# Optimization experiments

Hardware: AMD Instinct MI355X
Metric: run time of the kernel (lower is better)

Reference implementation:

```python
import jax, jax.numpy as jnp
import numpy as np

N = 20000
E = 320000
IN_C = 256
HID = 64
OUT_C = 64
NUM_LAYERS = 3
HEADS = 8


def setup_inputs() -> dict:
    key = jax.random.key(0)
    ks = jax.random.split(key, 12)
    s_in = 1.0 / np.sqrt(IN_C)
    s_h = 1.0 / np.sqrt(HID)
    inp = {
        "x": jax.random.normal(ks[0], (N, IN_C), dtype=jnp.float32),
        "edge_index": jax.random.randint(ks[1], (2, E), 0, N, dtype=jnp.int64),
        "lin1_w": jax.random.uniform(ks[2], (IN_C, HID), jnp.float32, -s_in, s_in),
        "lin1_b": jnp.zeros((HID,), jnp.float32),
        "wq": jax.random.uniform(ks[3], (NUM_LAYERS, HID, HID), jnp.float32, -s_h, s_h),
        "bq": jnp.zeros((NUM_LAYERS, HID), jnp.float32),
        "wk": jax.random.uniform(ks[4], (NUM_LAYERS, HID, HID), jnp.float32, -s_h, s_h),
        "bk": jnp.zeros((NUM_LAYERS, HID), jnp.float32),
        "wv": jax.random.uniform(ks[5], (NUM_LAYERS, HID, HID), jnp.float32, -s_h, s_h),
        "bv": jnp.zeros((NUM_LAYERS, HID), jnp.float32),
        "lin2_w": jax.random.uniform(ks[6], (HID, OUT_C), jnp.float32, -s_h, s_h),
        "lin2_b": jnp.zeros((OUT_C,), jnp.float32),
    }
    return inp


def reference(x, edge_index, lin1_w, lin1_b, wq, bq, wk, bk, wv, bv, lin2_w, lin2_b):
    n = x.shape[0]
    C = lin1_w.shape[1]
    d = C // HEADS  # per-head dim
    inv_sqrt_d = 1.0 / (d ** 0.5)

    # gcn_norm with self-loops (symmetric normalization, edge weights = 1)
    loop = jnp.arange(n, dtype=edge_index.dtype)
    row = jnp.concatenate([edge_index[0], loop])  # source j
    col = jnp.concatenate([edge_index[1], loop])  # target i
    deg = jax.ops.segment_sum(jnp.ones_like(col, dtype=x.dtype), col, num_segments=n)
    dinv = jnp.where(deg > 0, deg ** -0.5, 0.0)
    norm = dinv[row] * dinv[col]  # [E+N]

    # input projection (dropout inactive in eval mode)
    h = jax.nn.relu(x @ lin1_w + lin1_b)
    x_all = h[:, None, :]  # [N, 1, C] growing history

    for l in range(NUM_LAYERS):
        t = x_all.shape[1]
        # node-level projections (linear commutes with gather)
        q = x_all[:, -1] @ wq[l] + bq[l]                      # [N, C]
        k = jnp.einsum("ntc,cd->ntd", x_all, wk[l]) + bk[l]   # [N, t, C]
        v = jnp.einsum("ntc,cd->ntd", x_all, wv[l]) + bv[l]   # [N, t, C]
        # per-edge multi-head attention of target's latest repr over source history
        Qe = q[col].reshape(-1, HEADS, d)                      # [E', H, d]
        Ke = k[row].reshape(-1, t, HEADS, d)                   # [E', t, H, d]
        Ve = v[row].reshape(-1, t, HEADS, d)
        scores = jnp.einsum("ehd,ethd->eht", Qe, Ke) * inv_sqrt_d
        attn = jax.nn.softmax(scores, axis=-1)                 # [E', H, t]
        msg = jnp.einsum("eht,ethd->ehd", attn, Ve).reshape(-1, C)
        msg = msg * norm[:, None]
        out = jax.ops.segment_sum(msg, col, num_segments=n)    # sum aggregation
        out = jax.nn.relu(out)
        x_all = jnp.concatenate([x_all, out[:, None, :]], axis=1)

    logits = x_all[:, -1] @ lin2_w + lin2_b
    return jax.nn.log_softmax(logits, axis=1)
```

## Files before the change

### kernel.cpp

```cpp
#include <hip/hip_runtime.h>
#include <math.h>

#define HID 64
#define HEADS 8
#define ALD 72

typedef __attribute__((ext_vector_type(8))) short bf16x8;
typedef __attribute__((ext_vector_type(4))) float f32x4;

__device__ __forceinline__ unsigned short f2bf(float f) {
    union { float f; unsigned int u; } cv; cv.f = f;
    unsigned int u = cv.u;
    unsigned int r = (u + 0x7FFFu + ((u >> 16) & 1u)) >> 16;
    return (unsigned short)r;
}
__device__ __forceinline__ float bflo(unsigned int u) {
    union { unsigned int u; float f; } cv; cv.u = u << 16; return cv.f;
}
__device__ __forceinline__ float bfhi(unsigned int u) {
    union { unsigned int u; float f; } cv; cv.u = u & 0xFFFF0000u; return cv.f;
}
__device__ __forceinline__ unsigned relu_pk(unsigned u) {
    unsigned m = ((u & 0x8000u) ? 0u : 0xFFFFu) |
                 ((u & 0x80000000u) ? 0u : 0xFFFF0000u);
    return u & m;
}

__device__ __forceinline__ float dot8(const float* qp, uint4 u) {
    return qp[0] * bflo(u.x) + qp[1] * bfhi(u.x) + qp[2] * bflo(u.y) +
           qp[3] * bfhi(u.y) + qp[4] * bflo(u.z) + qp[5] * bfhi(u.z) +
           qp[6] * bflo(u.w) + qp[7] * bfhi(u.w);
}
__device__ __forceinline__ void axpy8(float a, uint4 u, float* Y) {
    Y[0] += a * bflo(u.x); Y[1] += a * bfhi(u.x);
    Y[2] += a * bflo(u.y); Y[3] += a * bfhi(u.y);
    Y[4] += a * bflo(u.z); Y[5] += a * bfhi(u.z);
    Y[6] += a * bflo(u.w); Y[7] += a * bfhi(u.w);
}

__global__ void k_count(const int* __restrict__ col, int* __restrict__ counts, int E) {
    int e = blockIdx.x * blockDim.x + threadIdx.x;
    if (e < E) atomicAdd(&counts[col[e]], 1);
}

__global__ __launch_bounds__(1024) void k_scan(const int* __restrict__ counts,
                                               int* __restrict__ start,
                                               float* __restrict__ dinv, int n) {
    __shared__ int wsum[16];
    int tid = threadIdx.x;
    int lane = tid & 63, wvi = tid >> 6;
    int ipt = (n + 1023) >> 10;
    int c0 = tid * ipt;
    int c1 = min(n, c0 + ipt);
    int s = 0;
    for (int i = c0; i < c1; ++i) s += counts[i];
    int x = s;
#pragma unroll
    for (int off = 1; off < 64; off <<= 1) {
        int y = __shfl_up(x, off);
        if (lane >= off) x += y;
    }
    if (lane == 63) wsum[wvi] = x;
    __syncthreads();
    if (wvi == 0 && lane < 16) {
        int t2 = wsum[lane];
#pragma unroll
        for (int off = 1; off < 16; off <<= 1) {
            int y = __shfl_up(t2, off);
            if (lane >= off) t2 += y;
        }
        wsum[lane] = t2;
    }
    __syncthreads();
    int waveoff = (wvi > 0) ? wsum[wvi - 1] : 0;
    int run = waveoff + x - s;
    for (int i = c0; i < c1; ++i) {
        int v = counts[i];
        start[i] = run;
        dinv[i] = rsqrtf((float)(v + 1));
        run += v;
    }
    if (tid == 0) start[n] = wsum[15];
}

__global__ void k_scatter(const int* __restrict__ ei, const int* __restrict__ start,
                          int* __restrict__ counts, unsigned short* __restrict__ ebuf,
                          int E) {
    int e = blockIdx.x * blockDim.x + threadIdx.x;
    if (e >= E) return;
    int r = ei[e], c = ei[E + e];
    int pos = start[c] + atomicSub(&counts[c], 1) - 1;
    ebuf[pos] = (unsigned short)r;
}

__device__ __forceinline__ void stage_w_bf16(unsigned short* Wt,
                                             const float* __restrict__ w, int tid) {
    for (int idx = tid; idx < 1024; idx += 256) {
        int k = idx >> 4, n4 = (idx & 15) * 4;
        float4 wv = *(const float4*)&w[k * 64 + n4];
        Wt[(n4 + 0) * ALD + k] = f2bf(wv.x);
        Wt[(n4 + 1) * ALD + k] = f2bf(wv.y);
        Wt[(n4 + 2) * ALD + k] = f2bf(wv.z);
        Wt[(n4 + 3) * ALD + k] = f2bf(wv.w);
    }
}

__device__ __forceinline__ void mfma_step(const unsigned short* Alds,
                                          const unsigned short* Wt,
                                          int tid, f32x4 acc[4]) {
    int lane = tid & 63;
    int m0 = (tid >> 6) * 16;
    int c16 = lane & 15, quad = lane >> 4;
    const unsigned short* ar = &Alds[(m0 + c16) * ALD + quad * 8];
    bf16x8 a0 = *(const bf16x8*)ar;
    bf16x8 a1 = *(const bf16x8*)(ar + 32);
#pragma unroll
    for (int nt = 0; nt < 4; ++nt) {
        const unsigned short* br = &Wt[(nt * 16 + c16) * ALD + quad * 8];
        bf16x8 b0 = *(const bf16x8*)br;
        bf16x8 b1 = *(const bf16x8*)(br + 32);
        acc[nt] = __builtin_amdgcn_mfma_f32_16x16x32_bf16(a0, b0, acc[nt], 0, 0, 0);
        acc[nt] = __builtin_amdgcn_mfma_f32_16x16x32_bf16(a1, b1, acc[nt], 0, 0, 0);
    }
}

__global__ __launch_bounds__(256, 4) void k_lin1(
    const float* __restrict__ x, const float* __restrict__ w,
    const float* __restrict__ b, const float* __restrict__ wv0,
    const float* __restrict__ bv0, unsigned short* __restrict__ h,
    unsigned short* __restrict__ kv, int n) {
    __shared__ __align__(16) unsigned short Alds[64 * ALD];
    __shared__ __align__(16) unsigned short Wt[64 * ALD];
    int tid = threadIdx.x;
    int node0 = blockIdx.x * 64;
    f32x4 acc[4];
#pragma unroll
    for (int nt = 0; nt < 4; ++nt) acc[nt] = (f32x4){0.f, 0.f, 0.f, 0.f};

    for (int kc = 0; kc < 256; kc += 64) {
        __syncthreads();
        stage_w_bf16(Wt, w + kc * 64, tid);
        for (int idx = tid; idx < 1024; idx += 256) {
            int r = idx >> 4, c4 = (idx & 15) * 4;
            int node = node0 + r;
            float4 v = make_float4(0.f, 0.f, 0.f, 0.f);
            if (node < n) v = *(const float4*)&x[(size_t)node * 256 + kc + c4];
            Alds[r * ALD + c4 + 0] = f2bf(v.x);
            Alds[r * ALD + c4 + 1] = f2bf(v.y);
            Alds[r * ALD + c4 + 2] = f2bf(v.z);
            Alds[r * ALD + c4 + 3] = f2bf(v.w);
        }
        __syncthreads();
        mfma_step(Alds, Wt, tid, acc);
    }
    int lane = tid & 63;
    int m0 = (tid >> 6) * 16, c16 = lane & 15, quad = lane >> 4;
    float bias[4];
#pragma unroll
    for (int nt = 0; nt < 4; ++nt) bias[nt] = b[nt * 16 + c16];

    __syncthreads();
    stage_w_bf16(Wt, wv0, tid);
#pragma unroll
    for (int i = 0; i < 4; ++i) {
        int row = m0 + quad * 4 + i;
        int node = node0 + row;
#pragma unroll
        for (int nt = 0; nt < 4; ++nt) {
            unsigned short hb = f2bf(fmaxf(acc[nt][i] + bias[nt], 0.f));
            Alds[row * ALD + nt * 16 + c16] = hb;
            if (node < n) h[(size_t)node * 64 + nt * 16 + c16] = hb;
        }
    }
    __syncthreads();
    f32x4 acc2[4];
#pragma unroll
    for (int nt = 0; nt < 4; ++nt) acc2[nt] = (f32x4){0.f, 0.f, 0.f, 0.f};
    mfma_step(Alds, Wt, tid, acc2);
    float bias2[4];
#pragma unroll
    for (int nt = 0; nt < 4; ++nt) bias2[nt] = bv0[nt * 16 + c16];
#pragma unroll
    for (int i = 0; i < 4; ++i) {
        int node = node0 + m0 + quad * 4 + i;
        if (node < n) {
#pragma unroll
            for (int nt = 0; nt < 4; ++nt)
                kv[(size_t)node * 64 + nt * 16 + c16] = f2bf(acc2[nt][i] + bias2[nt]);
        }
    }
}

__global__ __launch_bounds__(256, 4) void k_stage(
    const unsigned short* __restrict__ xs, size_t sstride,
    const float* __restrict__ wk, const float* __restrict__ bk,
    const float* __restrict__ wv, const float* __restrict__ bv,
    unsigned short* __restrict__ kv1, unsigned short* __restrict__ kv2,
    int n, int phase) {
    int j = blockIdx.y;
    int layer, s, isV;
    if (phase == 0) { layer = 1; s = j & 1; isV = j >> 1; }
    else            { layer = 2; s = j >> 1; isV = j & 1; }
    const unsigned short* src = xs + (size_t)s * sstride;
    const float* w = (isV ? wv : wk) + layer * 4096;
    const float* b = (isV ? bv : bk) + layer * 64;
    unsigned short* dst = (layer == 1) ? kv1 : kv2;
    int stride = (layer == 1) ? 256 : 384;
    int koff = s * 128 + (isV ? 64 : 0);
    bool relu_in = (s >= 1);

    __shared__ __align__(16) unsigned short Alds[64 * ALD];
    __shared__ __align__(16) unsigned short Wt[64 * ALD];
    int tid = threadIdx.x;
    int node0 = blockIdx.x * 64;
    stage_w_bf16(Wt, w, tid);
    for (int idx = tid; idx < 512; idx += 256) {
        int r = idx >> 3, seg = idx & 7;
        int node = node0 + r;
        uint4 u = make_uint4(0u, 0u, 0u, 0u);
        if (node < n) u = *(const uint4*)&src[(size_t)node * 64 + seg * 8];
        if (relu_in) {
            u.x = relu_pk(u.x); u.y = relu_pk(u.y);
            u.z = relu_pk(u.z); u.w = relu_pk(u.w);
        }
        *(uint4*)&Alds[r * ALD + seg * 8] = u;
    }
    __syncthreads();
    f32x4 acc[4];
#pragma unroll
    for (int nt = 0; nt < 4; ++nt) acc[nt] = (f32x4){0.f, 0.f, 0.f, 0.f};
    mfma_step(Alds, Wt, tid, acc);

    int lane = tid & 63;
    int m0 = (tid >> 6) * 16, c16 = lane & 15, quad = lane >> 4;
    float bias[4];
#pragma unroll
    for (int nt = 0; nt < 4; ++nt) bias[nt] = b[nt * 16 + c16];
#pragma unroll
    for (int i = 0; i < 4; ++i) {
        int node = node0 + m0 + quad * 4 + i;
        if (node < n) {
#pragma unroll
            for (int nt = 0; nt < 4; ++nt)
                dst[(size_t)node * stride + koff + nt * 16 + c16] =
                    f2bf(acc[nt][i] + bias[nt]);
        }
    }
}

template <int T, bool FINAL>
__global__ __launch_bounds__(256) void k_attn(
    const int* __restrict__ start, const unsigned short* __restrict__ ebuf,
    const float* __restrict__ dinv, const unsigned short* __restrict__ xs,
    size_t sstride, const unsigned short* __restrict__ kv,
    const float* __restrict__ wq, const float* __restrict__ bq,
    const float* __restrict__ w2, const float* __restrict__ b2,
    unsigned short* __restrict__ outb, float* __restrict__ outf, int n) {
    const int KVS = (T == 1) ? 64 : T * 128;
    int node = (int)((blockIdx.x * (size_t)blockDim.x + threadIdx.x) >> 6);
    int lane = threadIdx.x & 63;
    if (node >= n) return;
    int g = lane >> 3;
    int cb = (lane & 7) * 8;

    float qv[8];
    if (T > 1) {
        const float isd = 0.35355339059327373f;
        const unsigned short* xrow =
            &xs[(size_t)(T - 1) * sstride + (size_t)node * 64];
        float a0 = 0.f, a1 = 0.f, a2 = 0.f, a3 = 0.f;
        float a4 = 0.f, a5 = 0.f, a6 = 0.f, a7 = 0.f;
#pragma unroll
        for (int w8 = 0; w8 < 8; ++w8) {
            uint4 u = *(const uint4*)&xrow[w8 * 8];
            const float* wc = &wq[(w8 * 8) * 64 + lane];
            a0 += fmaxf(bflo(u.x), 0.f) * wc[0 * 64];
            a1 += fmaxf(bfhi(u.x), 0.f) * wc[1 * 64];
            a2 += fmaxf(bflo(u.y), 0.f) * wc[2 * 64];
            a3 += fmaxf(bfhi(u.y), 0.f) * wc[3 * 64];
            a4 += fmaxf(bflo(u.z), 0.f) * wc[4 * 64];
            a5 += fmaxf(bfhi(u.z), 0.f) * wc[5 * 64];
            a6 += fmaxf(bflo(u.w), 0.f) * wc[6 * 64];
            a7 += fmaxf(bfhi(u.w), 0.f) * wc[7 * 64];
        }
        float qo = bq[lane] + (((a0 + a1) + (a2 + a3)) + ((a4 + a5) + (a6 + a7)));
#pragma unroll
        for (int d = 0; d < 8; ++d) qv[d] = __shfl(qo, cb + d) * isd;
    }

    float dc = dinv[node];
    int s0 = start[node];
    int cnt = start[node + 1] - s0 + 1;

    float acc[8];
#pragma unroll
    for (int k = 0; k < 8; ++k) acc[k] = 0.f;

    int nch = (cnt + 7) >> 3;
    int idx = g;
    bool vc = idx < cnt;
    int rc = node;
    if (vc && idx > 0) rc = ebuf[s0 + idx - 1];
    float drc = vc ? dinv[rc] : 0.f;
    {
        const unsigned short* pc = kv + (size_t)rc * KVS;
        uint4 Kc[T], Vc[T];
#pragma unroll
        for (int s = 0; s < T; ++s) {
            if (T > 1) Kc[s] = *(const uint4*)&pc[s * 128 + cb];
            Vc[s] = *(const uint4*)&pc[((T == 1) ? 0 : s * 128 + 64) + cb];
        }

        for (int c = 0; c < nch; ++c) {
            int idxn = idx + 8;
            bool vn = idxn < cnt;
            int rn = node;
            if (vn) rn = ebuf[s0 + idxn - 1];
            float drn = vn ? dinv[rn] : 0.f;
            const unsigned short* pn = kv + (size_t)rn * KVS;
            uint4 Kn[T], Vn[T];
#pragma unroll
            for (int s = 0; s < T; ++s) {
                if (T > 1) Kn[s] = *(const uint4*)&pn[s * 128 + cb];
                Vn[s] = *(const uint4*)&pn[((T == 1) ? 0 : s * 128 + 64) + cb];
            }

            float sc[T];
            float wgt;
            if (T > 1) {
                float m = -1e30f;
#pragma unroll
                for (int s = 0; s < T; ++s) {
                    float p = dot8(qv, Kc[s]);
                    sc[s] = p;
                    m = fmaxf(m, p);
                }
                float denom = 0.f;
#pragma unroll
                for (int s = 0; s < T; ++s) {
                    sc[s] = __expf(sc[s] - m);
                    denom += sc[s];
                }
                wgt = drc / denom;
            } else {
                sc[0] = 1.f;
                wgt = drc;
            }

            float mg[8];
#pragma unroll
            for (int k = 0; k < 8; ++k) mg[k] = 0.f;
#pragma unroll
            for (int s = 0; s < T; ++s) axpy8(sc[s], Vc[s], mg);
#pragma unroll
            for (int k = 0; k < 8; ++k) acc[k] += wgt * mg[k];

#pragma unroll
            for (int s = 0; s < T; ++s) {
                if (T > 1) Kc[s] = Kn[s];
                Vc[s] = Vn[s];
            }
            drc = drn;
            idx = idxn;
        }
    }

#pragma unroll
    for (int off = 8; off < 64; off <<= 1) {
#pragma unroll
        for (int k = 0; k < 8; ++k) acc[k] += __shfl_xor(acc[k], off);
    }

    if (!FINAL) {
        if (g == 0) {
            ushort4 o0, o1;
            o0.x = f2bf(acc[0] * dc); o0.y = f2bf(acc[1] * dc);
            o0.z = f2bf(acc[2] * dc); o0.w = f2bf(acc[3] * dc);
            o1.x = f2bf(acc[4] * dc); o1.y = f2bf(acc[5] * dc);
            o1.z = f2bf(acc[6] * dc); o1.w = f2bf(acc[7] * dc);
            *(ushort4*)&outb[(size_t)node * 64 + cb] = o0;
            *(ushort4*)&outb[(size_t)node * 64 + cb + 4] = o1;
        }
    } else {
        float lg = b2[lane];
#pragma unroll
        for (int c = 0; c < 64; ++c) {
            float xc = fmaxf(__shfl(acc[c & 7], c >> 3) * dc, 0.f);
            lg += xc * w2[c * 64 + lane];
        }
        float mx = lg;
#pragma unroll
        for (int off = 1; off < 64; off <<= 1) mx = fmaxf(mx, __shfl_xor(mx, off));
        float e = __expf(lg - mx);
        float ssum = e;
#pragma unroll
        for (int off = 1; off < 64; off <<= 1) ssum += __shfl_xor(ssum, off);
        outf[(size_t)node * 64 + lane] = lg - mx - __logf(ssum);
    }
}

extern "C" void kernel_launch(void* const* d_in, const int* in_sizes, int n_in,
                              void* d_out, int out_size, void* d_ws, size_t ws_size,
                              hipStream_t stream) {
    const float* x  = (const float*)d_in[0];
    const int*   ei = (const int*)d_in[1];
    const float* w1 = (const float*)d_in[2];
    const float* b1 = (const float*)d_in[3];
    const float* wq = (const float*)d_in[4];
    const float* bq = (const float*)d_in[5];
    const float* wk = (const float*)d_in[6];
    const float* bk = (const float*)d_in[7];
    const float* wv = (const float*)d_in[8];
    const float* bv = (const float*)d_in[9];
    const float* w2 = (const float*)d_in[10];
    const float* b2 = (const float*)d_in[11];
    float* outp = (float*)d_out;

    int n = in_sizes[0] / 256;
    int E = in_sizes[1] / 2;

    float* ws = (float*)d_ws;
    size_t off = 0;
    float* dinv = ws + off; off += (size_t)n;
    unsigned short* xsU = (unsigned short*)(ws + off); off += (size_t)n * 96;
    unsigned short* kv0 = (unsigned short*)(ws + off); off += (size_t)n * 32;
    unsigned short* kv1 = (unsigned short*)(ws + off); off += (size_t)n * 128;
    unsigned short* kv2 = (unsigned short*)(ws + off); off += (size_t)n * 192;
    int* wsI    = (int*)(ws + off);
    int* counts = wsI;
    int* startA = wsI + n;
    unsigned short* ebuf = (unsigned short*)(wsI + 2 * n + 1);

    size_t sstride = (size_t)n * 64;

    hipMemsetAsync(counts, 0, (size_t)n * sizeof(int), stream);
    k_count<<<(E + 255) / 256, 256, 0, stream>>>(ei + E, counts, E);
    k_scan<<<1, 1024, 0, stream>>>(counts, startA, dinv, n);
    k_scatter<<<(E + 255) / 256, 256, 0, stream>>>(ei, startA, counts, ebuf, E);

    k_lin1<<<(n + 63) / 64, 256, 0, stream>>>(x, w1, b1, wv, bv, xsU, kv0, n);

    int attn_grid = (int)(((size_t)n * 64 + 255) / 256);
    int NT = (n + 63) / 64;

    k_attn<1, false><<<attn_grid, 256, 0, stream>>>(
        startA, ebuf, dinv, xsU, sstride, kv0, nullptr, nullptr, nullptr, nullptr,
        xsU + sstride, nullptr, n);

    {
        dim3 grid(NT, 4);
        k_stage<<<grid, 256, 0, stream>>>(xsU, sstride, wk, bk, wv, bv,
                                          kv1, kv2, n, 0);
    }
    k_attn<2, false><<<attn_grid, 256, 0, stream>>>(
        startA, ebuf, dinv, xsU, sstride, kv1, wq + 4096, bq + 64, nullptr, nullptr,
        xsU + 2 * sstride, nullptr, n);

    {
        dim3 grid(NT, 6);
        k_stage<<<grid, 256, 0, stream>>>(xsU, sstride, wk, bk, wv, bv,
                                          kv1, kv2, n, 1);
    }
    k_attn<3, true><<<attn_grid, 256, 0, stream>>>(
        startA, ebuf, dinv, xsU, sstride, kv2, wq + 8192, bq + 128, w2, b2,
        nullptr, outp, n);
}
```

Measured before the change: 269.5 us.

## Deepen edge-index prefetch, use bf16 dot2 for scores, fold softmax weights into accumulation

The attention kernel now prefetches source indices two chunks ahead, with branch-free index loads, and adds a scheduling barrier so the next chunk's K/V loads are issued before compute. Query vectors are packed to bf16 pairs and scores are computed with v_dot2_f32_bf16 instead of scalar unpack-and-multiply. Softmax weights are folded directly into the accumulator, dropping the intermediate message buffer. The aim is to hide gather latency and cut ALU work, at the cost of rounding the query to bf16, which changes numerics slightly.

```diff
diff --git a/kernel.cpp b/kernel.cpp
--- a/kernel.cpp
+++ b/kernel.cpp
@@ -26,11 +26,12 @@
     return u & m;
 }
 
-__device__ __forceinline__ float dot8(const float* qp, uint4 u) {
-    return qp[0] * bflo(u.x) + qp[1] * bfhi(u.x) + qp[2] * bflo(u.y) +
-           qp[3] * bfhi(u.y) + qp[4] * bflo(u.z) + qp[5] * bfhi(u.z) +
-           qp[6] * bflo(u.w) + qp[7] * bfhi(u.w);
-}
+__device__ __forceinline__ float dot2bf(unsigned a, unsigned b, float c) {
+    float d;
+    asm("v_dot2_f32_bf16 %0, %1, %2, %3" : "=v"(d) : "v"(a), "v"(b), "v"(c));
+    return d;
+}
+
 __device__ __forceinline__ void axpy8(float a, uint4 u, float* Y) {
     Y[0] += a * bflo(u.x); Y[1] += a * bfhi(u.x);
     Y[2] += a * bflo(u.y); Y[3] += a * bfhi(u.y);
@@ -248,6 +249,14 @@
     }
 }
 
+__device__ __forceinline__ int load_r(const unsigned short* __restrict__ ebuf,
+                                      int s0, int idx, int cnt, int node) {
+    bool e = (idx > 0) & (idx < cnt);
+    int a = e ? (s0 + idx - 1) : 0;
+    int r = ebuf[a];
+    return e ? r : node;
+}
+
 template <int T, bool FINAL>
 __global__ __launch_bounds__(256) void k_attn(
     const int* __restrict__ start, const unsigned short* __restrict__ ebuf,
@@ -263,7 +272,7 @@
     int g = lane >> 3;
     int cb = (lane & 7) * 8;
 
-    float qv[8];
+    unsigned qpk[4];
     if (T > 1) {
         const float isd = 0.35355339059327373f;
         const unsigned short* xrow =
@@ -285,7 +294,11 @@
         }
         float qo = bq[lane] + (((a0 + a1) + (a2 + a3)) + ((a4 + a5) + (a6 + a7)));
 #pragma unroll
-        for (int d = 0; d < 8; ++d) qv[d] = __shfl(qo, cb + d) * isd;
+        for (int j = 0; j < 4; ++j) {
+            float lo = __shfl(qo, cb + 2 * j) * isd;
+            float hi = __shfl(qo, cb + 2 * j + 1) * isd;
+            qpk[j] = ((unsigned)f2bf(hi) << 16) | (unsigned)f2bf(lo);
+        }
     }
 
     float dc = dinv[node];
@@ -297,72 +310,67 @@
     for (int k = 0; k < 8; ++k) acc[k] = 0.f;
 
     int nch = (cnt + 7) >> 3;
-    int idx = g;
-    bool vc = idx < cnt;
-    int rc = node;
-    if (vc && idx > 0) rc = ebuf[s0 + idx - 1];
-    float drc = vc ? dinv[rc] : 0.f;
+
+    int r_c = load_r(ebuf, s0, g, cnt, node);
+    int r_n = load_r(ebuf, s0, 8 + g, cnt, node);
+    float d0 = dinv[r_c];
+    float dr_c = (g < cnt) ? d0 : 0.f;
+    uint4 Kc[T], Vc[T];
     {
-        const unsigned short* pc = kv + (size_t)rc * KVS;
-        uint4 Kc[T], Vc[T];
+        const unsigned short* pc = kv + (size_t)r_c * KVS;
 #pragma unroll
         for (int s = 0; s < T; ++s) {
             if (T > 1) Kc[s] = *(const uint4*)&pc[s * 128 + cb];
             Vc[s] = *(const uint4*)&pc[((T == 1) ? 0 : s * 128 + 64) + cb];
         }
-
-        for (int c = 0; c < nch; ++c) {
-            int idxn = idx + 8;
-            bool vn = idxn < cnt;
-            int rn = node;
-            if (vn) rn = ebuf[s0 + idxn - 1];
-            float drn = vn ? dinv[rn] : 0.f;
-            const unsigned short* pn = kv + (size_t)rn * KVS;
-            uint4 Kn[T], Vn[T];
+    }
+
+    for (int c = 0; c < nch; ++c) {
+        int r_2 = load_r(ebuf, s0, (c + 2) * 8 + g, cnt, node);
+        float dn = dinv[r_n];
+        bool vn = ((c + 1) * 8 + g) < cnt;
+        float dr_n = vn ? dn : 0.f;
+        const unsigned short* pn = kv + (size_t)r_n * KVS;
+        uint4 Kn[T], Vn[T];
+#pragma unroll
+        for (int s = 0; s < T; ++s) {
+            if (T > 1) Kn[s] = *(const uint4*)&pn[s * 128 + cb];
+            Vn[s] = *(const uint4*)&pn[((T == 1) ? 0 : s * 128 + 64) + cb];
+        }
+        __builtin_amdgcn_sched_barrier(0);
+
+        float cf[T];
+        if (T > 1) {
+            float sc[T];
+            float m = -1e30f;
 #pragma unroll
             for (int s = 0; s < T; ++s) {
-                if (T > 1) Kn[s] = *(const uint4*)&pn[s * 128 + cb];
-                Vn[s] = *(const uint4*)&pn[((T == 1) ? 0 : s * 128 + 64) + cb];
+                float p = dot2bf(qpk[3], Kc[s].w,
+                          dot2bf(qpk[2], Kc[s].z,
+                          dot2bf(qpk[1], Kc[s].y,
+                          dot2bf(qpk[0], Kc[s].x, 0.f))));
+                sc[s] = p;
+                m = fmaxf(m, p);
             }
-
-            float sc[T];
-            float wgt;
-            if (T > 1) {
-                float m = -1e30f;
-#pragma unroll
-                for (int s = 0; s < T; ++s) {
-                    float p = dot8(qv, Kc[s]);
-                    sc[s] = p;
-                    m = fmaxf(m, p);
-                }
-                float denom = 0.f;
-#pragma unroll
-                for (int s = 0; s < T; ++s) {
-                    sc[s] = __expf(sc[s] - m);
-                    denom += sc[s];
-                }
-                wgt = drc / denom;
-            } else {
-                sc[0] = 1.f;
-                wgt = drc;
-            }
-
-            float mg[8];
-#pragma unroll
-            for (int k = 0; k < 8; ++k) mg[k] = 0.f;
-#pragma unroll
-            for (int s = 0; s < T; ++s) axpy8(sc[s], Vc[s], mg);
-#pragma unroll
-            for (int k = 0; k < 8; ++k) acc[k] += wgt * mg[k];
-
-#pragma unroll
-            for (int s = 0; s < T; ++s) {
-                if (T > 1) Kc[s] = Kn[s];
-                Vc[s] = Vn[s];
-            }
-            drc = drn;
-            idx = idxn;
-        }
+            float denom = 0.f;
+#pragma unroll
+            for (int s = 0; s < T; ++s) { sc[s] = __expf(sc[s] - m); denom += sc[s]; }
+            float w = dr_c / denom;
+#pragma unroll
+            for (int s = 0; s < T; ++s) cf[s] = w * sc[s];
+        } else {
+            cf[0] = dr_c;
+        }
+#pragma unroll
+        for (int s = 0; s < T; ++s) axpy8(cf[s], Vc[s], acc);
+
+#pragma unroll
+        for (int s = 0; s < T; ++s) {
+            if (T > 1) Kc[s] = Kn[s];
+            Vc[s] = Vn[s];
+        }
+        dr_c = dr_n;
+        r_n = r_2;
     }
 
 #pragma unroll
```

Result: slower. 277.9 us (+3.1%).
